# Kernel optimization log

Measured on AMD Instinct MI355X. Metric: run time of the kernel, lower is better.

## Reference

```python
import jax, jax.numpy as jnp
import numpy as np

EPS = 1e-6

def layernorm(x, alpha, bias):
    # torch.std default is unbiased (ddof=1)
    mean = x.mean(axis=-1, keepdims=True)
    std = jnp.std(x, axis=-1, keepdims=True, ddof=1)
    return alpha * (x - mean) / (std + EPS) + bias


def setup_inputs() -> dict:
    key = jax.random.key(0)
    B, L, d_model = 2, 1024, 1024
    d_state, d_conv, expand = 16, 4, 2
    d_inner = expand * d_model
    ks = jax.random.split(key, 8)
    std = 0.02
    x = jax.random.normal(ks[0], (B, L, d_model), dtype=jnp.float32)
    in_proj_w = jax.random.normal(ks[1], (2 * d_inner, d_model), dtype=jnp.float32) * std
    in_proj_b = jnp.zeros((2 * d_inner,), jnp.float32)
    conv_w = jax.random.normal(ks[2], (d_inner, 1, d_conv), dtype=jnp.float32) * std  # depthwise, groups=d_inner
    conv_b = jnp.zeros((d_inner,), jnp.float32)
    x_proj_w = jax.random.normal(ks[3], (2 * d_state, d_inner), dtype=jnp.float32) * std
    x_proj_b = jnp.zeros((2 * d_state,), jnp.float32)
    dt_proj_w = jax.random.normal(ks[4], (d_inner, d_inner), dtype=jnp.float32) * std
    dt_proj_b = jnp.zeros((d_inner,), jnp.float32)
    A_log = jnp.log(jnp.tile(jnp.arange(1, d_state + 1, dtype=jnp.float32), (d_inner, 1)))
    D = jnp.ones((d_inner,), jnp.float32)
    out_proj_w = jax.random.normal(ks[5], (d_model, d_inner), dtype=jnp.float32) * std
    out_proj_b = jnp.zeros((d_model,), jnp.float32)
    in_norm_alpha = jnp.ones((d_model,), jnp.float32)
    in_norm_bias = jnp.zeros((d_model,), jnp.float32)
    norm_alpha = jnp.ones((d_model,), jnp.float32)
    norm_bias = jnp.zeros((d_model,), jnp.float32)
    return {"x": x, "in_proj_w": in_proj_w, "in_proj_b": in_proj_b,
            "conv_w": conv_w, "conv_b": conv_b,
            "x_proj_w": x_proj_w, "x_proj_b": x_proj_b,
            "dt_proj_w": dt_proj_w, "dt_proj_b": dt_proj_b,
            "A_log": A_log, "D": D,
            "out_proj_w": out_proj_w, "out_proj_b": out_proj_b,
            "in_norm_alpha": in_norm_alpha, "in_norm_bias": in_norm_bias,
            "norm_alpha": norm_alpha, "norm_bias": norm_bias}


def reference(x, in_proj_w, in_proj_b, conv_w, conv_b, x_proj_w, x_proj_b,
              dt_proj_w, dt_proj_b, A_log, D, out_proj_w, out_proj_b,
              in_norm_alpha, in_norm_bias, norm_alpha, norm_bias):
    batch, L, d_model = x.shape
    d_inner = D.shape[0]
    d_state = A_log.shape[1]
    d_conv = conv_w.shape[-1]

    residual = x
    xn = layernorm(x, in_norm_alpha, in_norm_bias)
    xz = xn @ in_proj_w.T + in_proj_b                    # (B, L, 2*d_inner)
    x_in, z = jnp.split(xz, 2, axis=-1)

    # causal depthwise conv: torch pads both sides by d_conv-1 then slices [:L]
    # -> equivalent to left-pad only
    xc = jnp.swapaxes(x_in, 1, 2)                        # (B, d_inner, L)
    xc = jax.lax.conv_general_dilated(
        xc, conv_w, window_strides=(1,), padding=[(d_conv - 1, 0)],
        dimension_numbers=('NCH', 'OIH', 'NCH'),
        feature_group_count=d_inner) + conv_b[None, :, None]
    xc = jax.nn.silu(jnp.swapaxes(xc, 1, 2))             # (B, L, d_inner)

    Bmat, Cmat = jnp.split(xc @ x_proj_w.T + x_proj_b, 2, axis=-1)  # (B, L, d_state) each
    delta = jnp.clip(jax.nn.softplus(xc @ dt_proj_w.T + dt_proj_b), 1e-4, 10.0)
    A = -jnp.exp(A_log)                                  # (d_inner, d_state)
    flags = (jnp.arange(L) % 16) == 15                   # periodic renorm mask

    def step(h, inp):
        d_t, B_t, C_t, x_t, flag = inp                   # d_t,x_t: (B,d_inner); B_t,C_t: (B,d_state)
        dA = jnp.exp(jnp.clip(d_t[..., None] * A, -10.0, 0.0))      # (B,d_inner,d_state)
        dBx = d_t[..., None] * B_t[:, None, :] * x_t[..., None]
        h = dA * h + dBx
        hn = jnp.maximum(jnp.linalg.norm(h, axis=-1, keepdims=True), 1e-6)
        scale = jnp.where(hn > 10.0, 10.0 / hn, 1.0)
        h = jnp.where(flag, h * scale, h)
        y_t = jnp.sum(C_t[:, None, :] * h, axis=-1) + D * x_t
        return h, y_t

    h0 = jnp.zeros((batch, d_inner, d_state), dtype=x.dtype)
    xs = (jnp.swapaxes(delta, 0, 1), jnp.swapaxes(Bmat, 0, 1),
          jnp.swapaxes(Cmat, 0, 1), jnp.swapaxes(xc, 0, 1), flags)
    _, ys = jax.lax.scan(step, h0, xs)                   # ys: (L, B, d_inner)
    y = jnp.swapaxes(ys, 0, 1)

    y = y * jax.nn.silu(z)
    out = y @ out_proj_w.T + out_proj_b                  # dropout is identity in eval
    return layernorm(residual + out, norm_alpha, norm_bias)
```

## Files before the change

### kernel.cpp

```cpp
#include <hip/hip_runtime.h>
#include <math.h>

typedef unsigned short u16;
typedef unsigned int   u32;
typedef __bf16 bf16x8 __attribute__((ext_vector_type(8)));
typedef float  f32x4  __attribute__((ext_vector_type(4)));
typedef u16    u16x8  __attribute__((ext_vector_type(8)));

#define NB   2
#define LL   1024
#define DM   1024
#define DI   2048
#define MM   (NB*LL)
#define NXZ  (2*DI)
#define DSTATE 16
#define NSEG 64
#define NDT  2176
#define F32PAT 0x3F800000u

__device__ __forceinline__ float b2f(u16 u) {
  union { u32 i; float f; } v; v.i = ((u32)u) << 16; return v.f;
}
__device__ __forceinline__ u16 f2b(float f) {
  union { float f; u32 i; } v; v.f = f;
  u32 r = (v.i + 0x7FFFu + ((v.i >> 16) & 1u)) >> 16;
  return (u16)r;
}
__device__ __forceinline__ float ldx(const void* p, size_t i, bool isf32) {
  return isf32 ? ((const float*)p)[i] : b2f(((const u16*)p)[i]);
}
__device__ __forceinline__ float spclip(float v) {
  v = (v > 20.0f) ? v : __logf(1.0f + __expf(v));
  return fminf(fmaxf(v, 1e-4f), 10.0f);
}

typedef __attribute__((address_space(1))) const void gas_t;
typedef __attribute__((address_space(3))) void las_t;
__device__ __forceinline__ void gload_lds16(const void* g, void* l) {
  __builtin_amdgcn_global_load_lds((gas_t*)g, (las_t*)l, 16, 0, 0);
}

#define CVT_A  4194304u
#define CVT_B  8388608u
#define CVT_C 10485760u
#define CVT_D 10551296u
#define CVT_E 10747904u
#define CVT_BLOCKS 10496

__global__ __launch_bounds__(256) void cvtln_kernel(
    const void* __restrict__ s_in, const void* __restrict__ s_dt,
    const void* __restrict__ s_op, const void* __restrict__ s_xp,
    u16* __restrict__ inpw, u16* __restrict__ wdt, u16* __restrict__ opw,
    const void* __restrict__ x, const void* __restrict__ alpha,
    const void* __restrict__ beta, u16* __restrict__ xn,
    const u32* __restrict__ probe)
{
  const bool isf32 = (*probe == F32PAT);
  __shared__ float sb[4], ssb[4];
  if (blockIdx.x < CVT_BLOCKS) {
    size_t i4 = ((size_t)blockIdx.x * 256 + threadIdx.x) * 4;
    const void* src; u16* dst; size_t off;
    if      (i4 < CVT_A) { src = s_in; dst = inpw;        off = i4; }
    else if (i4 < CVT_B) { src = s_dt; dst = wdt;         off = i4 - CVT_A; }
    else if (i4 < CVT_C) { src = s_op; dst = opw;         off = i4 - CVT_B; }
    else if (i4 < CVT_D) { src = s_xp; dst = wdt + CVT_A; off = i4 - CVT_C; }
    else {
      ushort4 z = {0, 0, 0, 0};
      *(ushort4*)(wdt + 4259840u + (i4 - CVT_D)) = z;
      return;
    }
    ushort4 o;
    if (isf32) {
      float4 f = *(const float4*)((const float*)src + off);
      o.x = f2b(f.x); o.y = f2b(f.y); o.z = f2b(f.z); o.w = f2b(f.w);
    } else {
      o = *(const ushort4*)((const u16*)src + off);
    }
    *(ushort4*)(dst + off) = o;
    return;
  }
  int row = blockIdx.x - CVT_BLOCKS;
  int base = threadIdx.x * 4;
  size_t ix = (size_t)row * DM + base;
  float v0, v1, v2, v3;
  if (isf32) {
    float4 f = *(const float4*)((const float*)x + ix);
    v0 = f.x; v1 = f.y; v2 = f.z; v3 = f.w;
  } else {
    ushort4 u = *(const ushort4*)((const u16*)x + ix);
    v0 = b2f(u.x); v1 = b2f(u.y); v2 = b2f(u.z); v3 = b2f(u.w);
  }
  float s  = v0 + v1 + v2 + v3;
  float ss = v0*v0 + v1*v1 + v2*v2 + v3*v3;
#pragma unroll
  for (int off = 32; off > 0; off >>= 1) {
    s  += __shfl_down(s,  off);
    ss += __shfl_down(ss, off);
  }
  int wv = threadIdx.x >> 6, ln = threadIdx.x & 63;
  if (ln == 0) { sb[wv] = s; ssb[wv] = ss; }
  __syncthreads();
  s  = sb[0]  + sb[1]  + sb[2]  + sb[3];
  ss = ssb[0] + ssb[1] + ssb[2] + ssb[3];
  float mean = s * (1.0f / DM);
  float var  = fmaxf((ss - (float)DM * mean * mean) * (1.0f / (DM - 1)), 0.0f);
  float inv  = 1.0f / (sqrtf(var) + 1e-6f);
  float a0 = ldx(alpha, base+0, isf32), a1 = ldx(alpha, base+1, isf32);
  float a2 = ldx(alpha, base+2, isf32), a3 = ldx(alpha, base+3, isf32);
  float b0 = ldx(beta,  base+0, isf32), b1 = ldx(beta,  base+1, isf32);
  float b2 = ldx(beta,  base+2, isf32), b3 = ldx(beta,  base+3, isf32);
  ushort4 o;
  o.x = f2b(a0 * (v0 - mean) * inv + b0);
  o.y = f2b(a1 * (v1 - mean) * inv + b1);
  o.z = f2b(a2 * (v2 - mean) * inv + b2);
  o.w = f2b(a3 * (v3 - mean) * inv + b3);
  *(ushort4*)(xn + ix) = o;
}

__global__ __launch_bounds__(256) void ln1_kernel(
    const void* __restrict__ x, const void* __restrict__ alpha,
    const void* __restrict__ beta, u16* __restrict__ out,
    const u32* __restrict__ probe)
{
  const bool isf32 = (*probe == F32PAT);
  int row = blockIdx.x;
  int base = threadIdx.x * 4;
  size_t ix = (size_t)row * DM + base;
  float v0, v1, v2, v3;
  if (isf32) {
    float4 f = *(const float4*)((const float*)x + ix);
    v0 = f.x; v1 = f.y; v2 = f.z; v3 = f.w;
  } else {
    ushort4 u = *(const ushort4*)((const u16*)x + ix);
    v0 = b2f(u.x); v1 = b2f(u.y); v2 = b2f(u.z); v3 = b2f(u.w);
  }
  float s  = v0 + v1 + v2 + v3;
  float ss = v0*v0 + v1*v1 + v2*v2 + v3*v3;
#pragma unroll
  for (int off = 32; off > 0; off >>= 1) {
    s  += __shfl_down(s,  off);
    ss += __shfl_down(ss, off);
  }
  __shared__ float sb[4], ssb[4];
  int wv = threadIdx.x >> 6, ln = threadIdx.x & 63;
  if (ln == 0) { sb[wv] = s; ssb[wv] = ss; }
  __syncthreads();
  s  = sb[0]  + sb[1]  + sb[2]  + sb[3];
  ss = ssb[0] + ssb[1] + ssb[2] + ssb[3];
  float mean = s * (1.0f / DM);
  float var  = fmaxf((ss - (float)DM * mean * mean) * (1.0f / (DM - 1)), 0.0f);
  float inv  = 1.0f / (sqrtf(var) + 1e-6f);
  float a0 = ldx(alpha, base+0, isf32), a1 = ldx(alpha, base+1, isf32);
  float a2 = ldx(alpha, base+2, isf32), a3 = ldx(alpha, base+3, isf32);
  float b0 = ldx(beta,  base+0, isf32), b1 = ldx(beta,  base+1, isf32);
  float b2 = ldx(beta,  base+2, isf32), b3 = ldx(beta,  base+3, isf32);
  ushort4 o;
  o.x = f2b(a0 * (v0 - mean) * inv + b0);
  o.y = f2b(a1 * (v1 - mean) * inv + b1);
  o.z = f2b(a2 * (v2 - mean) * inv + b2);
  o.w = f2b(a3 * (v3 - mean) * inv + b3);
  *(ushort4*)(out + ix) = o;
}

__global__ __launch_bounds__(256) void ln2_kernel(
    const void* __restrict__ x, const float* __restrict__ outp,
    const void* __restrict__ alpha, const void* __restrict__ beta,
    void* __restrict__ out, const u32* __restrict__ probe)
{
  const bool isf32 = (*probe == F32PAT);
  int row = blockIdx.x;
  int base = threadIdx.x * 4;
  size_t ix = (size_t)row * DM + base;
  float v0, v1, v2, v3;
  if (isf32) {
    float4 f = *(const float4*)((const float*)x + ix);
    v0 = f.x; v1 = f.y; v2 = f.z; v3 = f.w;
  } else {
    ushort4 u = *(const ushort4*)((const u16*)x + ix);
    v0 = b2f(u.x); v1 = b2f(u.y); v2 = b2f(u.z); v3 = b2f(u.w);
  }
  float4 p = *(const float4*)(outp + ix);
  v0 += p.x; v1 += p.y; v2 += p.z; v3 += p.w;
  float s  = v0 + v1 + v2 + v3;
  float ss = v0*v0 + v1*v1 + v2*v2 + v3*v3;
#pragma unroll
  for (int off = 32; off > 0; off >>= 1) {
    s  += __shfl_down(s,  off);
    ss += __shfl_down(ss, off);
  }
  __shared__ float sb[4], ssb[4];
  int wv = threadIdx.x >> 6, ln = threadIdx.x & 63;
  if (ln == 0) { sb[wv] = s; ssb[wv] = ss; }
  __syncthreads();
  s  = sb[0]  + sb[1]  + sb[2]  + sb[3];
  ss = ssb[0] + ssb[1] + ssb[2] + ssb[3];
  float mean = s * (1.0f / DM);
  float var  = fmaxf((ss - (float)DM * mean * mean) * (1.0f / (DM - 1)), 0.0f);
  float inv  = 1.0f / (sqrtf(var) + 1e-6f);
  float a0 = ldx(alpha, base+0, isf32), a1 = ldx(alpha, base+1, isf32);
  float a2 = ldx(alpha, base+2, isf32), a3 = ldx(alpha, base+3, isf32);
  float b0 = ldx(beta,  base+0, isf32), b1 = ldx(beta,  base+1, isf32);
  float b2 = ldx(beta,  base+2, isf32), b3 = ldx(beta,  base+3, isf32);
  float r0 = a0 * (v0 - mean) * inv + b0;
  float r1 = a1 * (v1 - mean) * inv + b1;
  float r2 = a2 * (v2 - mean) * inv + b2;
  float r3 = a3 * (v3 - mean) * inv + b3;
  if (isf32) {
    float4 o; o.x = r0; o.y = r1; o.z = r2; o.w = r3;
    *(float4*)((float*)out + ix) = o;
  } else {
    ushort4 o; o.x = f2b(r0); o.y = f2b(r1); o.z = f2b(r2); o.w = f2b(r3);
    *(ushort4*)((u16*)out + ix) = o;
  }
}

__global__ __launch_bounds__(256) void ln2_sk_kernel(
    const void* __restrict__ x, const float* __restrict__ P,
    const void* __restrict__ op_bias,
    const void* __restrict__ alpha, const void* __restrict__ beta,
    void* __restrict__ out, const u32* __restrict__ probe)
{
  const bool isf32 = (*probe == F32PAT);
  int row = blockIdx.x;
  int base = threadIdx.x * 4;
  size_t ix = (size_t)row * DM + base;
  float v0, v1, v2, v3;
  if (isf32) {
    float4 f = *(const float4*)((const float*)x + ix);
    v0 = f.x; v1 = f.y; v2 = f.z; v3 = f.w;
  } else {
    ushort4 u = *(const ushort4*)((const u16*)x + ix);
    v0 = b2f(u.x); v1 = b2f(u.y); v2 = b2f(u.z); v3 = b2f(u.w);
  }
  v0 += ldx(op_bias, base+0, isf32);
  v1 += ldx(op_bias, base+1, isf32);
  v2 += ldx(op_bias, base+2, isf32);
  v3 += ldx(op_bias, base+3, isf32);
#pragma unroll
  for (int sk = 0; sk < 4; ++sk) {
    float4 p = *(const float4*)(P + ((size_t)sk * MM + row) * DM + base);
    v0 += p.x; v1 += p.y; v2 += p.z; v3 += p.w;
  }
  float s  = v0 + v1 + v2 + v3;
  float ss = v0*v0 + v1*v1 + v2*v2 + v3*v3;
#pragma unroll
  for (int off = 32; off > 0; off >>= 1) {
    s  += __shfl_down(s,  off);
    ss += __shfl_down(ss, off);
  }
  __shared__ float sb[4], ssb[4];
  int wv = threadIdx.x >> 6, ln = threadIdx.x & 63;
  if (ln == 0) { sb[wv] = s; ssb[wv] = ss; }
  __syncthreads();
  s  = sb[0]  + sb[1]  + sb[2]  + sb[3];
  ss = ssb[0] + ssb[1] + ssb[2] + ssb[3];
  float mean = s * (1.0f / DM);
  float var  = fmaxf((ss - (float)DM * mean * mean) * (1.0f / (DM - 1)), 0.0f);
  float inv  = 1.0f / (sqrtf(var) + 1e-6f);
  float a0 = ldx(alpha, base+0, isf32), a1 = ldx(alpha, base+1, isf32);
  float a2 = ldx(alpha, base+2, isf32), a3 = ldx(alpha, base+3, isf32);
  float b0 = ldx(beta,  base+0, isf32), b1 = ldx(beta,  base+1, isf32);
  float b2 = ldx(beta,  base+2, isf32), b3 = ldx(beta,  base+3, isf32);
  float r0 = a0 * (v0 - mean) * inv + b0;
  float r1 = a1 * (v1 - mean) * inv + b1;
  float r2 = a2 * (v2 - mean) * inv + b2;
  float r3 = a3 * (v3 - mean) * inv + b3;
  if (isf32) {
    float4 o; o.x = r0; o.y = r1; o.z = r2; o.w = r3;
    *(float4*)((float*)out + ix) = o;
  } else {
    ushort4 o; o.x = f2b(r0); o.y = f2b(r1); o.z = f2b(r2); o.w = f2b(r3);
    *(ushort4*)((u16*)out + ix) = o;
  }
}

__global__ __launch_bounds__(256) void cvt_kernel(
    const void* __restrict__ s_in, const void* __restrict__ s_dt,
    const void* __restrict__ s_op, const void* __restrict__ s_xp,
    u16* __restrict__ inpw, u16* __restrict__ wdt, u16* __restrict__ opw,
    const u32* __restrict__ probe)
{
  const bool isf32 = (*probe == F32PAT);
  size_t i4 = ((size_t)blockIdx.x * 256 + threadIdx.x) * 4;
  if (i4 >= CVT_E) return;
  const void* src; u16* dst; size_t off;
  if      (i4 < CVT_A) { src = s_in; dst = inpw;        off = i4; }
  else if (i4 < CVT_B) { src = s_dt; dst = wdt;         off = i4 - CVT_A; }
  else if (i4 < CVT_C) { src = s_op; dst = opw;         off = i4 - CVT_B; }
  else if (i4 < CVT_D) { src = s_xp; dst = wdt + CVT_A; off = i4 - CVT_C; }
  else {
    ushort4 z = {0, 0, 0, 0};
    *(ushort4*)(wdt + 4259840u + (i4 - CVT_D)) = z;
    return;
  }
  ushort4 o;
  if (isf32) {
    float4 f = *(const float4*)((const float*)src + off);
    o.x = f2b(f.x); o.y = f2b(f.y); o.z = f2b(f.z); o.w = f2b(f.w);
  } else {
    o = *(const ushort4*)((const u16*)src + off);
  }
  *(ushort4*)(dst + off) = o;
}

__device__ __forceinline__ void stage64(const u16* __restrict__ G, int rowK,
                                        int k0, u16* __restrict__ lds,
                                        int wave, int lane, int m0) {
#pragma unroll
  for (int q = 0; q < 4; ++q) {
    int ci = (wave * 4 + q) * 64 + lane;
    int r  = ci >> 3;
    int s  = ci & 7;
    int ch = s ^ (r & 7);
    const u16* ga = G + (size_t)(m0 + r) * rowK + k0 + ch * 8;
    gload_lds16(ga, lds + (size_t)ci * 8);
  }
}
__device__ __forceinline__ bf16x8 frag64(const u16* __restrict__ lds,
                                         int r, int ch) {
  int s = ch ^ (r & 7);
  return *(const bf16x8*)(lds + (size_t)r * 64 + s * 8);
}

#define EPI_NONE 0
#define EPI_SOFTPLUS 1

template<int EPI, int OUTBF>
__global__ __launch_bounds__(256) void gemm_fast(
    const u16* __restrict__ A, const u16* __restrict__ W,
    const void* __restrict__ bias, void* __restrict__ Cout,
    const u32* __restrict__ probe, int M, int N, int K)
{
  __shared__ __align__(16) u16 As[128 * 64];
  __shared__ __align__(16) u16 Ws[128 * 64];
  const bool isf32 = (*probe == F32PAT);
  const int tid  = threadIdx.x;
  const int wave = tid >> 6;
  const int lane = tid & 63;
  const int quad = lane >> 4;
  const int l16  = lane & 15;
  const int m0 = blockIdx.x * 128;
  const int n0 = blockIdx.y * 128;
  const int wm = (wave >> 1) * 64;
  const int wn = (wave & 1) * 64;

  f32x4 acc[4][4] = {};

  for (int k0 = 0; k0 < K; k0 += 64) {
    __syncthreads();
    stage64(A, K, k0, As, wave, lane, m0);
    stage64(W, K, k0, Ws, wave, lane, n0);
    __syncthreads();
#pragma unroll
    for (int kk = 0; kk < 2; ++kk) {
      bf16x8 af[4], bfr[4];
#pragma unroll
      for (int i = 0; i < 4; ++i) {
        af[i]  = frag64(As, wm + i * 16 + l16, kk * 4 + quad);
        bfr[i] = frag64(Ws, wn + i * 16 + l16, kk * 4 + quad);
      }
#pragma unroll
      for (int i = 0; i < 4; ++i)
#pragma unroll
        for (int j = 0; j < 4; ++j)
          acc[i][j] = __builtin_amdgcn_mfma_f32_16x16x32_bf16(af[i], bfr[j], acc[i][j], 0, 0, 0);
    }
  }

#pragma unroll
  for (int i = 0; i < 4; ++i) {
    int rbase = m0 + wm + i * 16 + quad * 4;
#pragma unroll
    for (int j = 0; j < 4; ++j) {
      int col = n0 + wn + j * 16 + l16;
      float bv = ldx(bias, col, isf32);
#pragma unroll
      for (int r = 0; r < 4; ++r) {
        float v = acc[i][j][r] + bv;
        if (EPI == EPI_SOFTPLUS) v = spclip(v);
        size_t oi = (size_t)(rbase + r) * N + col;
        if (OUTBF) ((u16*)Cout)[oi] = f2b(v);
        else       ((float*)Cout)[oi] = v;
      }
    }
  }
}

template<int PARTBF>
__global__ __launch_bounds__(256) void gemm_sk(
    const u16* __restrict__ A, const u16* __restrict__ W,
    void* __restrict__ P, int M, int N, int Kfull, int Kslice)
{
  __shared__ __align__(16) u16 As[128 * 64];
  __shared__ __align__(16) u16 Ws[128 * 64];
  const int tid  = threadIdx.x;
  const int wave = tid >> 6;
  const int lane = tid & 63;
  const int quad = lane >> 4;
  const int l16  = lane & 15;
  const int m0 = blockIdx.x * 128;
  const int n0 = blockIdx.y * 128;
  const int sk = blockIdx.z;
  const int kbeg = sk * Kslice;
  const int kend = kbeg + Kslice;
  const int wm = (wave >> 1) * 64;
  const int wn = (wave & 1) * 64;

  f32x4 acc[4][4] = {};

  for (int k0 = kbeg; k0 < kend; k0 += 64) {
    __syncthreads();
    stage64(A, Kfull, k0, As, wave, lane, m0);
    stage64(W, Kfull, k0, Ws, wave, lane, n0);
    __syncthreads();
#pragma unroll
    for (int kk = 0; kk < 2; ++kk) {
      bf16x8 af[4], bfr[4];
#pragma unroll
      for (int i = 0; i < 4; ++i) {
        af[i]  = frag64(As, wm + i * 16 + l16, kk * 4 + quad);
        bfr[i] = frag64(Ws, wn + i * 16 + l16, kk * 4 + quad);
      }
#pragma unroll
      for (int i = 0; i < 4; ++i)
#pragma unroll
        for (int j = 0; j < 4; ++j)
          acc[i][j] = __builtin_amdgcn_mfma_f32_16x16x32_bf16(af[i], bfr[j], acc[i][j], 0, 0, 0);
    }
  }

#pragma unroll
  for (int i = 0; i < 4; ++i) {
    int rbase = m0 + wm + i * 16 + quad * 4;
#pragma unroll
    for (int j = 0; j < 4; ++j) {
      int col = n0 + wn + j * 16 + l16;
#pragma unroll
      for (int r = 0; r < 4; ++r) {
        size_t oi = (size_t)sk * M * N + (size_t)(rbase + r) * N + col;
        if (PARTBF) ((u16*)P)[oi] = f2b(acc[i][j][r]);
        else        ((float*)P)[oi] = acc[i][j][r];
      }
    }
  }
}

template<int EPI, int OUTBF>
__global__ __launch_bounds__(256) void gemm_r2(
    const u16* __restrict__ A, const void* __restrict__ W,
    const void* __restrict__ bias, void* __restrict__ Cout,
    const u32* __restrict__ probe, int M, int N, int K)
{
  __shared__ __align__(16) u16 As[128 * 32];
  __shared__ __align__(16) u16 Ws[128 * 32];
  const bool isf32 = (*probe == F32PAT);
  const int tid  = threadIdx.x;
  const int wave = tid >> 6;
  const int lane = tid & 63;
  const int quad = lane >> 4;
  const int l16  = lane & 15;
  const int m0 = blockIdx.x * 128;
  const int n0 = blockIdx.y * 128;
  const int wm = (wave >> 1) * 64;
  const int wn = (wave & 1) * 64;

  f32x4 acc[4][4] = {};

  for (int k0 = 0; k0 < K; k0 += 32) {
    u16x8 va[2], vw[2];
#pragma unroll
    for (int q = 0; q < 2; ++q) {
      int ci  = wave * 128 + q * 64 + lane;
      int row = ci >> 2;
      int kc  = (ci & 3) * 8;
      va[q] = *(const u16x8*)(A + (size_t)(m0 + row) * K + k0 + kc);
      size_t wi = (size_t)(n0 + row) * K + k0 + kc;
      if (isf32) {
        const float* Wf = (const float*)W;
        float4 f0 = *(const float4*)(Wf + wi);
        float4 f1 = *(const float4*)(Wf + wi + 4);
        u16x8 t;
        t[0] = f2b(f0.x); t[1] = f2b(f0.y); t[2] = f2b(f0.z); t[3] = f2b(f0.w);
        t[4] = f2b(f1.x); t[5] = f2b(f1.y); t[6] = f2b(f1.z); t[7] = f2b(f1.w);
        vw[q] = t;
      } else {
        vw[q] = *(const u16x8*)((const u16*)W + wi);
      }
    }
    __syncthreads();
#pragma unroll
    for (int q = 0; q < 2; ++q) {
      int ci = wave * 128 + q * 64 + lane;
      *(u16x8*)(As + (size_t)ci * 8) = va[q];
      *(u16x8*)(Ws + (size_t)ci * 8) = vw[q];
    }
    __syncthreads();
    bf16x8 af[4], bfr[4];
#pragma unroll
    for (int i = 0; i < 4; ++i) {
      af[i]  = *(const bf16x8*)(As + (size_t)(wm + i * 16 + l16) * 32 + quad * 8);
      bfr[i] = *(const bf16x8*)(Ws + (size_t)(wn + i * 16 + l16) * 32 + quad * 8);
    }
#pragma unroll
    for (int i = 0; i < 4; ++i)
#pragma unroll
      for (int j = 0; j < 4; ++j)
        acc[i][j] = __builtin_amdgcn_mfma_f32_16x16x32_bf16(af[i], bfr[j], acc[i][j], 0, 0, 0);
  }

#pragma unroll
  for (int i = 0; i < 4; ++i) {
    int rbase = m0 + wm + i * 16 + quad * 4;
#pragma unroll
    for (int j = 0; j < 4; ++j) {
      int col = n0 + wn + j * 16 + l16;
      float bv = ldx(bias, col, isf32);
#pragma unroll
      for (int r = 0; r < 4; ++r) {
        float v = acc[i][j][r] + bv;
        if (EPI == EPI_SOFTPLUS) v = spclip(v);
        size_t oi = (size_t)(rbase + r) * N + col;
        if (OUTBF) ((u16*)Cout)[oi] = f2b(v);
        else       ((float*)Cout)[oi] = v;
      }
    }
  }
}

__global__ __launch_bounds__(256) void conv_silu_kernel(
    const u16* __restrict__ xz, const void* __restrict__ cw,
    const void* __restrict__ cb, u16* __restrict__ xc_bf,
    const u32* __restrict__ probe)
{
  const bool isf32 = (*probe == F32PAT);
  int g = blockIdx.x * 256 + threadIdx.x;
  int c = g & (DI - 1);
  int m = g >> 11;
  int l = m & (LL - 1);
  float w0 = ldx(cw, c*4+0, isf32), w1 = ldx(cw, c*4+1, isf32);
  float w2 = ldx(cw, c*4+2, isf32), w3 = ldx(cw, c*4+3, isf32);
  const u16* col = xz + (size_t)m * NXZ + c;
  float acc = ldx(cb, c, isf32);
  acc += w3 * b2f(col[0]);
  if (l >= 1) acc += w2 * b2f(*(col - NXZ));
  if (l >= 2) acc += w1 * b2f(*(col - 2*NXZ));
  if (l >= 3) acc += w0 * b2f(*(col - 3*NXZ));
  float sil = acc / (1.0f + __expf(-acc));
  xc_bf[g] = f2b(sil);
}

__global__ __launch_bounds__(256) void proj_bc_r2(
    const u16* __restrict__ xc, const void* __restrict__ W,
    const void* __restrict__ bias, float* __restrict__ bc,
    const u32* __restrict__ probe)
{
  const bool isf32 = (*probe == F32PAT);
  int m = blockIdx.x;
  int n = threadIdx.x >> 3;
  int part = threadIdx.x & 7;
  const u16* xr = xc + (size_t)m * DI + part * 256;
  size_t wbase = (size_t)n * DI + part * 256;
  float acc = 0.0f;
  if (isf32) {
    const float* wr = (const float*)W + wbase;
#pragma unroll 8
    for (int i = 0; i < 256; i += 4) {
      ushort4 xv = *(const ushort4*)(xr + i);
      float4  wv = *(const float4*)(wr + i);
      acc += b2f(xv.x)*wv.x + b2f(xv.y)*wv.y + b2f(xv.z)*wv.z + b2f(xv.w)*wv.w;
    }
  } else {
    const u16* wr = (const u16*)W + wbase;
#pragma unroll 8
    for (int i = 0; i < 256; i += 4) {
      ushort4 xv = *(const ushort4*)(xr + i);
      ushort4 wv = *(const ushort4*)(wr + i);
      acc += b2f(xv.x)*b2f(wv.x) + b2f(xv.y)*b2f(wv.y)
           + b2f(xv.z)*b2f(wv.z) + b2f(xv.w)*b2f(wv.w);
    }
  }
  __shared__ float ps[256];
  ps[threadIdx.x] = acc;
  __syncthreads();
  if (threadIdx.x < 32) {
    float s = 0.0f;
#pragma unroll
    for (int p = 0; p < 8; ++p) s += ps[threadIdx.x * 8 + p];
    bc[(size_t)m * 32 + threadIdx.x] = s + ldx(bias, threadIdx.x, isf32);
  }
}

__global__ __launch_bounds__(256, 4) void scan_p1(
    const u16* __restrict__ Pdt, const void* __restrict__ bias_dt,
    const void* __restrict__ bias_xp,
    const u16* __restrict__ xc, const void* __restrict__ A_log,
    float2* __restrict__ PQ, const u32* __restrict__ probe)
{
  const bool isf32 = (*probe == F32PAT);
  const int c = blockIdx.x * 256 + threadIdx.x;
  const int g = blockIdx.y;
  const int b = blockIdx.z;
  const int row0 = b * LL + g * 16;
  const u16* P0 = Pdt;
  const u16* P1 = Pdt + (size_t)MM * NDT;
  __shared__ float sBC[512];
  if (threadIdx.x < 128) {
    int j = threadIdx.x >> 3, k0 = (threadIdx.x & 7) * 4;
    size_t base = (size_t)(row0 + j) * NDT + DI + k0;
#pragma unroll
    for (int i = 0; i < 4; ++i)
      sBC[j * 32 + k0 + i] = b2f(P0[base + i]) + b2f(P1[base + i])
                           + ldx(bias_xp, k0 + i, isf32);
  }
  float Av2[16];
#pragma unroll
  for (int s = 0; s < 16; ++s)
    Av2[s] = -__expf(ldx(A_log, (size_t)c * DSTATE + s, isf32)) * 1.44269504f;
  const float bdt = ldx(bias_dt, c, isf32);
  float p[16], q[16];
#pragma unroll
  for (int s = 0; s < 16; ++s) { p[s] = 1.0f; q[s] = 0.0f; }
  __syncthreads();
  const float CLIP2 = -14.4269504f;
#pragma unroll 4
  for (int j = 0; j < 16; ++j) {
    int row = row0 + j;
    size_t pi = (size_t)row * NDT + c;
    float d  = spclip(b2f(P0[pi]) + b2f(P1[pi]) + bdt);
    float x  = b2f(xc[(size_t)row * DI + c]);
    float dx = d * x;
    float4 B4[4];
    B4[0] = *(const float4*)&sBC[j * 32 + 0];
    B4[1] = *(const float4*)&sBC[j * 32 + 4];
    B4[2] = *(const float4*)&sBC[j * 32 + 8];
    B4[3] = *(const float4*)&sBC[j * 32 + 12];
    const float* Bv = (const float*)B4;
#pragma unroll
    for (int s = 0; s < 16; ++s) {
      float a = __builtin_amdgcn_exp2f(fmaxf(d * Av2[s], CLIP2));
      q[s] = a * q[s] + dx * Bv[s];
      p[s] *= a;
    }
  }
  float2* out = PQ + ((size_t)(b * NSEG + g) * DI + c) * DSTATE;
#pragma unroll
  for (int s = 0; s < 16; ++s) out[s] = make_float2(p[s], q[s]);
}

__global__ __launch_bounds__(256) void scan_p2(
    const float2* __restrict__ PQ, u16* __restrict__ Hin,
    float* __restrict__ Scale)
{
  const int s = threadIdx.x & 15;
  const int c = blockIdx.x * 16 + (threadIdx.x >> 4);
  const int b = blockIdx.y;
  const size_t stride = (size_t)DI * DSTATE;
  const size_t base = ((size_t)b * NSEG * DI + c) * DSTATE + s;
  float h = 0.0f;
  float2 pq = PQ[base];
  for (int g = 0; g < NSEG; ++g) {
    float2 cur = pq;
    if (g < NSEG - 1) pq = PQ[base + (size_t)(g + 1) * stride];
    Hin[base + (size_t)g * stride] = f2b(h);
    h = cur.x * h + cur.y;
    float n2 = h * h;
    n2 += __shfl_xor(n2, 1);
    n2 += __shfl_xor(n2, 2);
    n2 += __shfl_xor(n2, 4);
    n2 += __shfl_xor(n2, 8);
    float hn = fmaxf(sqrtf(n2), 1e-6f);
    float sc = hn > 10.0f ? 10.0f / hn : 1.0f;
    if (s == 0) Scale[((size_t)b * NSEG + g) * DI + c] = sc;
    h *= sc;
  }
}

__global__ __launch_bounds__(256, 4) void scan_p3(
    const u16* __restrict__ Pdt, const void* __restrict__ bias_dt,
    const void* __restrict__ bias_xp,
    const u16* __restrict__ xc, const u16* __restrict__ xz,
    const void* __restrict__ A_log, const void* __restrict__ Dp,
    const u16* __restrict__ Hin, const float* __restrict__ Scale,
    u16* __restrict__ y_bf, const u32* __restrict__ probe)
{
  const bool isf32 = (*probe == F32PAT);
  const int c = blockIdx.x * 256 + threadIdx.x;
  const int g = blockIdx.y;
  const int b = blockIdx.z;
  const int row0 = b * LL + g * 16;
  const u16* P0 = Pdt;
  const u16* P1 = Pdt + (size_t)MM * NDT;
  __shared__ float sBC[512];
  if (threadIdx.x < 128) {
    int j = threadIdx.x >> 3, k0 = (threadIdx.x & 7) * 4;
    size_t base = (size_t)(row0 + j) * NDT + DI + k0;
#pragma unroll
    for (int i = 0; i < 4; ++i)
      sBC[j * 32 + k0 + i] = b2f(P0[base + i]) + b2f(P1[base + i])
                           + ldx(bias_xp, k0 + i, isf32);
  }
  float Av2[16];
#pragma unroll
  for (int s = 0; s < 16; ++s)
    Av2[s] = -__expf(ldx(A_log, (size_t)c * DSTATE + s, isf32)) * 1.44269504f;
  const float bdt = ldx(bias_dt, c, isf32);
  float h[16];
  const u16* hp = Hin + ((size_t)(b * NSEG + g) * DI + c) * DSTATE;
  {
    u16x8 h0 = *(const u16x8*)(hp);
    u16x8 h1 = *(const u16x8*)(hp + 8);
#pragma unroll
    for (int s = 0; s < 8; ++s) { h[s] = b2f(h0[s]); h[8 + s] = b2f(h1[s]); }
  }
  const float sc15 = Scale[((size_t)b * NSEG + g) * DI + c];
  const float Dc = ldx(Dp, c, isf32);
  __syncthreads();
  const float CLIP2 = -14.4269504f;
#pragma unroll 4
  for (int j = 0; j < 16; ++j) {
    int row = row0 + j;
    size_t pi = (size_t)row * NDT + c;
    float d  = spclip(b2f(P0[pi]) + b2f(P1[pi]) + bdt);
    float x  = b2f(xc[(size_t)row * DI + c]);
    float z  = b2f(xz[(size_t)row * NXZ + DI + c]);
    float dx = d * x;
    float4 BC[8];
    BC[0] = *(const float4*)&sBC[j * 32 + 0];
    BC[1] = *(const float4*)&sBC[j * 32 + 4];
    BC[2] = *(const float4*)&sBC[j * 32 + 8];
    BC[3] = *(const float4*)&sBC[j * 32 + 12];
    BC[4] = *(const float4*)&sBC[j * 32 + 16];
    BC[5] = *(const float4*)&sBC[j * 32 + 20];
    BC[6] = *(const float4*)&sBC[j * 32 + 24];
    BC[7] = *(const float4*)&sBC[j * 32 + 28];
    const float* Bv = (const float*)BC;
    const float* Cv = Bv + 16;
#pragma unroll
    for (int s = 0; s < 16; ++s) {
      float a = __builtin_amdgcn_exp2f(fmaxf(d * Av2[s], CLIP2));
      h[s] = a * h[s] + dx * Bv[s];
    }
    if (j == 15) {
#pragma unroll
      for (int s = 0; s < 16; ++s) h[s] *= sc15;
    }
    float ys = 0.0f;
#pragma unroll
    for (int s = 0; s < 16; ++s) ys += Cv[s] * h[s];
    float yo = (ys + Dc * x) * (z / (1.0f + __expf(-z)));
    y_bf[(size_t)row * DI + c] = f2b(yo);
  }
}

__global__ __launch_bounds__(256) void scan_mono(
    const float* __restrict__ delta, const float* __restrict__ bc,
    const u16* __restrict__ xc, const u16* __restrict__ xz,
    const void* __restrict__ A_log, const void* __restrict__ Dp,
    u16* __restrict__ y_bf, const u32* __restrict__ probe)
{
  const bool isf32 = (*probe == F32PAT);
  const int s = threadIdx.x & 15;
  const int c = blockIdx.x * 16 + (threadIdx.x >> 4);
  const int b = blockIdx.y;
  const float Av2 = -__expf(ldx(A_log, (size_t)c * DSTATE + s, isf32)) * 1.44269504f;
  const float Dc  = ldx(Dp, c, isf32);
  const float CLIP2 = -14.4269504f;
  float h = 0.0f;
  for (int t0 = 0; t0 < LL; t0 += 16) {
    float dl[16], xl[16], zl[16], Bv[16], Cv[16];
#pragma unroll
    for (int j = 0; j < 16; ++j) {
      int row = b * LL + t0 + j;
      dl[j] = delta[(size_t)row * DI + c];
      xl[j] = b2f(xc[(size_t)row * DI + c]);
      zl[j] = b2f(xz[(size_t)row * NXZ + DI + c]);
      Bv[j] = bc[(size_t)row * 32 + s];
      Cv[j] = bc[(size_t)row * 32 + 16 + s];
    }
#pragma unroll
    for (int j = 0; j < 16; ++j) {
      float d = dl[j], x = xl[j];
      float dA = __builtin_amdgcn_exp2f(fmaxf(d * Av2, CLIP2));
      h = dA * h + (d * x) * Bv[j];
      if (j == 15) {
        float n2 = h * h;
        n2 += __shfl_xor(n2, 1); n2 += __shfl_xor(n2, 2);
        n2 += __shfl_xor(n2, 4); n2 += __shfl_xor(n2, 8);
        float hn = fmaxf(sqrtf(n2), 1e-6f);
        float sc = hn > 10.0f ? 10.0f / hn : 1.0f;
        h *= sc;
      }
      float ys = Cv[j] * h;
      ys += __shfl_xor(ys, 1); ys += __shfl_xor(ys, 2);
      ys += __shfl_xor(ys, 4); ys += __shfl_xor(ys, 8);
      float z = zl[j];
      float yo = (ys + Dc * x) * (z / (1.0f + __expf(-z)));
      if (s == 0) {
        int row = b * LL + t0 + j;
        y_bf[(size_t)row * DI + c] = f2b(yo);
      }
    }
  }
}

extern "C" void kernel_launch(void* const* d_in, const int* in_sizes, int n_in,
                              void* d_out, int out_size, void* d_ws, size_t ws_size,
                              hipStream_t stream) {
  const void* x          = d_in[0];
  const void* in_proj_w  = d_in[1];
  const void* in_proj_b  = d_in[2];
  const void* conv_w     = d_in[3];
  const void* conv_b     = d_in[4];
  const void* x_proj_w   = d_in[5];
  const void* x_proj_b   = d_in[6];
  const void* dt_proj_w  = d_in[7];
  const void* dt_proj_b  = d_in[8];
  const void* A_log      = d_in[9];
  const void* Dp         = d_in[10];
  const void* out_proj_w = d_in[11];
  const void* out_proj_b = d_in[12];
  const void* in_norm_a  = d_in[13];
  const void* in_norm_b  = d_in[14];
  const void* norm_a     = d_in[15];
  const void* norm_b     = d_in[16];
  const u32*  probe      = (const u32*)d_in[13];

  const size_t MiB = 1048576;
  const size_t NEED_NEW = 106299392;

  if (ws_size >= NEED_NEW) {
    char* w = (char*)d_ws;
    u16*   xz_bf = (u16*)w;    w += 16 * MiB;
    u16*   xc_bf = (u16*)w;    w += 8 * MiB;
    u16*   Pdt   = (u16*)w;    w += 17 * MiB;
    float* Scale = (float*)w;  w += 1 * MiB;
    u16*   opw   = (u16*)w;    w += 4 * MiB;
    u16*   y_bf  = (u16*)w;    w += 8 * MiB;
    char* S = w;
    u16*    inpw   = (u16*)(S);
    u16*    wdt    = (u16*)(S + 8*MiB);
    u16*    xn_bf  = (u16*)(S + 16*MiB + 512*1024);
    float2* PQ     = (float2*)(S);
    u16*    Hin    = (u16*)(S + 32*MiB);
    float*  outP   = (float*)(S);

    cvtln_kernel<<<CVT_BLOCKS + MM, 256, 0, stream>>>(
        in_proj_w, dt_proj_w, out_proj_w, x_proj_w, inpw, wdt, opw,
        x, in_norm_a, in_norm_b, xn_bf, probe);
    gemm_fast<EPI_NONE, 1><<<dim3(MM/128, NXZ/128), 256, 0, stream>>>(
        xn_bf, inpw, in_proj_b, xz_bf, probe, MM, NXZ, DM);
    conv_silu_kernel<<<(MM * DI) / 256, 256, 0, stream>>>(xz_bf, conv_w, conv_b, xc_bf, probe);
    gemm_sk<1><<<dim3(MM/128, NDT/128, 2), 256, 0, stream>>>(
        xc_bf, wdt, Pdt, MM, NDT, DI, DI/2);
    scan_p1<<<dim3(DI/256, NSEG, NB), 256, 0, stream>>>(
        Pdt, dt_proj_b, x_proj_b, xc_bf, A_log, PQ, probe);
    scan_p2<<<dim3(DI/16, NB), 256, 0, stream>>>(PQ, Hin, Scale);
    scan_p3<<<dim3(DI/256, NSEG, NB), 256, 0, stream>>>(
        Pdt, dt_proj_b, x_proj_b, xc_bf, xz_bf, A_log, Dp, Hin, Scale, y_bf, probe);
    gemm_sk<0><<<dim3(MM/128, DM/128, 4), 256, 0, stream>>>(
        y_bf, opw, outP, MM, DM, DI, DI/4);
    ln2_sk_kernel<<<MM, 256, 0, stream>>>(x, outP, out_proj_b, norm_a, norm_b, d_out, probe);
  } else {
    char* w = (char*)d_ws;
    u16*   xn_bf = (u16*)w;   w += (size_t)MM * DM * 2;
    u16*   xz_bf = (u16*)w;   w += (size_t)MM * NXZ * 2;
    u16*   xc_bf = (u16*)w;   w += (size_t)MM * DI * 2;
    float* delta = (float*)w; w += (size_t)MM * DI * 4;
    float* bc    = (float*)w; w += (size_t)MM * 32 * 4;
    u16*   y_bf  = (u16*)w;   w += (size_t)MM * DI * 2;
    float* outp  = (float*)w; w += (size_t)MM * DM * 4;

    ln1_kernel<<<MM, 256, 0, stream>>>(x, in_norm_a, in_norm_b, xn_bf, probe);
    gemm_r2<EPI_NONE, 1><<<dim3(MM/128, NXZ/128), 256, 0, stream>>>(
        xn_bf, in_proj_w, in_proj_b, xz_bf, probe, MM, NXZ, DM);
    conv_silu_kernel<<<(MM * DI) / 256, 256, 0, stream>>>(xz_bf, conv_w, conv_b, xc_bf, probe);
    gemm_r2<EPI_SOFTPLUS, 0><<<dim3(MM/128, DI/128), 256, 0, stream>>>(
        xn_bf == 0 ? xc_bf : xc_bf, dt_proj_w, dt_proj_b, delta, probe, MM, DI, DI);
    proj_bc_r2<<<MM, 256, 0, stream>>>(xc_bf, x_proj_w, x_proj_b, bc, probe);
    scan_mono<<<dim3(DI/16, NB), 256, 0, stream>>>(delta, bc, xc_bf, xz_bf, A_log, Dp, y_bf, probe);
    gemm_r2<EPI_NONE, 0><<<dim3(MM/128, DM/128), 256, 0, stream>>>(
        y_bf, out_proj_w, out_proj_b, outp, probe, MM, DM, DI);
    ln2_kernel<<<MM, 256, 0, stream>>>(x, outp, norm_a, norm_b, d_out, probe);
  }
}
```

Before: 315.1 us.

## Split-K all GEMMs with bf16 partials and fold bias into consumers

Replaces the in_proj GEMM with a 2-way split-K GEMM that writes bf16 partial planes. The conv and scan_p3 kernels now sum those partials and add the in_proj bias themselves. The dt/x_proj GEMM goes from 2-way to 4-way split-K, and out_proj partials are stored as bf16 instead of fp32 before the final layernorm sums them. The aim is more blocks in flight for the 16x16-tile GEMMs and less partial-buffer traffic. In exchange, consumers read more partial planes, the workspace requirement grows to 172 MiB, and bf16 rounding of partials may reduce accuracy.

```diff
diff --git a/kernel.cpp b/kernel.cpp
--- a/kernel.cpp
+++ b/kernel.cpp
@@ -214,8 +214,8 @@
   }
 }
 
-__global__ __launch_bounds__(256) void ln2_sk_kernel(
-    const void* __restrict__ x, const float* __restrict__ P,
+__global__ __launch_bounds__(256) void ln2_skb_kernel(
+    const void* __restrict__ x, const u16* __restrict__ P,
     const void* __restrict__ op_bias,
     const void* __restrict__ alpha, const void* __restrict__ beta,
     void* __restrict__ out, const u32* __restrict__ probe)
@@ -238,8 +238,8 @@
   v3 += ldx(op_bias, base+3, isf32);
 #pragma unroll
   for (int sk = 0; sk < 4; ++sk) {
-    float4 p = *(const float4*)(P + ((size_t)sk * MM + row) * DM + base);
-    v0 += p.x; v1 += p.y; v2 += p.z; v3 += p.w;
+    ushort4 p = *(const ushort4*)(P + ((size_t)sk * MM + row) * DM + base);
+    v0 += b2f(p.x); v1 += b2f(p.y); v2 += b2f(p.z); v3 += b2f(p.w);
   }
   float s  = v0 + v1 + v2 + v3;
   float ss = v0*v0 + v1*v1 + v2*v2 + v3*v3;
@@ -274,35 +274,6 @@
   }
 }
 
-__global__ __launch_bounds__(256) void cvt_kernel(
-    const void* __restrict__ s_in, const void* __restrict__ s_dt,
-    const void* __restrict__ s_op, const void* __restrict__ s_xp,
-    u16* __restrict__ inpw, u16* __restrict__ wdt, u16* __restrict__ opw,
-    const u32* __restrict__ probe)
-{
-  const bool isf32 = (*probe == F32PAT);
-  size_t i4 = ((size_t)blockIdx.x * 256 + threadIdx.x) * 4;
-  if (i4 >= CVT_E) return;
-  const void* src; u16* dst; size_t off;
-  if      (i4 < CVT_A) { src = s_in; dst = inpw;        off = i4; }
-  else if (i4 < CVT_B) { src = s_dt; dst = wdt;         off = i4 - CVT_A; }
-  else if (i4 < CVT_C) { src = s_op; dst = opw;         off = i4 - CVT_B; }
-  else if (i4 < CVT_D) { src = s_xp; dst = wdt + CVT_A; off = i4 - CVT_C; }
-  else {
-    ushort4 z = {0, 0, 0, 0};
-    *(ushort4*)(wdt + 4259840u + (i4 - CVT_D)) = z;
-    return;
-  }
-  ushort4 o;
-  if (isf32) {
-    float4 f = *(const float4*)((const float*)src + off);
-    o.x = f2b(f.x); o.y = f2b(f.y); o.z = f2b(f.z); o.w = f2b(f.w);
-  } else {
-    o = *(const ushort4*)((const u16*)src + off);
-  }
-  *(ushort4*)(dst + off) = o;
-}
-
 __device__ __forceinline__ void stage64(const u16* __restrict__ G, int rowK,
                                         int k0, u16* __restrict__ lds,
                                         int wave, int lane, int m0) {
@@ -322,74 +293,9 @@
   return *(const bf16x8*)(lds + (size_t)r * 64 + s * 8);
 }
 
-#define EPI_NONE 0
-#define EPI_SOFTPLUS 1
-
-template<int EPI, int OUTBF>
-__global__ __launch_bounds__(256) void gemm_fast(
-    const u16* __restrict__ A, const u16* __restrict__ W,
-    const void* __restrict__ bias, void* __restrict__ Cout,
-    const u32* __restrict__ probe, int M, int N, int K)
-{
-  __shared__ __align__(16) u16 As[128 * 64];
-  __shared__ __align__(16) u16 Ws[128 * 64];
-  const bool isf32 = (*probe == F32PAT);
-  const int tid  = threadIdx.x;
-  const int wave = tid >> 6;
-  const int lane = tid & 63;
-  const int quad = lane >> 4;
-  const int l16  = lane & 15;
-  const int m0 = blockIdx.x * 128;
-  const int n0 = blockIdx.y * 128;
-  const int wm = (wave >> 1) * 64;
-  const int wn = (wave & 1) * 64;
-
-  f32x4 acc[4][4] = {};
-
-  for (int k0 = 0; k0 < K; k0 += 64) {
-    __syncthreads();
-    stage64(A, K, k0, As, wave, lane, m0);
-    stage64(W, K, k0, Ws, wave, lane, n0);
-    __syncthreads();
-#pragma unroll
-    for (int kk = 0; kk < 2; ++kk) {
-      bf16x8 af[4], bfr[4];
-#pragma unroll
-      for (int i = 0; i < 4; ++i) {
-        af[i]  = frag64(As, wm + i * 16 + l16, kk * 4 + quad);
-        bfr[i] = frag64(Ws, wn + i * 16 + l16, kk * 4 + quad);
-      }
-#pragma unroll
-      for (int i = 0; i < 4; ++i)
-#pragma unroll
-        for (int j = 0; j < 4; ++j)
-          acc[i][j] = __builtin_amdgcn_mfma_f32_16x16x32_bf16(af[i], bfr[j], acc[i][j], 0, 0, 0);
-    }
-  }
-
-#pragma unroll
-  for (int i = 0; i < 4; ++i) {
-    int rbase = m0 + wm + i * 16 + quad * 4;
-#pragma unroll
-    for (int j = 0; j < 4; ++j) {
-      int col = n0 + wn + j * 16 + l16;
-      float bv = ldx(bias, col, isf32);
-#pragma unroll
-      for (int r = 0; r < 4; ++r) {
-        float v = acc[i][j][r] + bv;
-        if (EPI == EPI_SOFTPLUS) v = spclip(v);
-        size_t oi = (size_t)(rbase + r) * N + col;
-        if (OUTBF) ((u16*)Cout)[oi] = f2b(v);
-        else       ((float*)Cout)[oi] = v;
-      }
-    }
-  }
-}
-
-template<int PARTBF>
 __global__ __launch_bounds__(256) void gemm_sk(
     const u16* __restrict__ A, const u16* __restrict__ W,
-    void* __restrict__ P, int M, int N, int Kfull, int Kslice)
+    u16* __restrict__ P, int M, int N, int Kfull, int Kslice)
 {
   __shared__ __align__(16) u16 As[128 * 64];
   __shared__ __align__(16) u16 Ws[128 * 64];
@@ -429,6 +335,7 @@
     }
   }
 
+  u16* Pb = P + (size_t)sk * M * N;
 #pragma unroll
   for (int i = 0; i < 4; ++i) {
     int rbase = m0 + wm + i * 16 + quad * 4;
@@ -436,14 +343,14 @@
     for (int j = 0; j < 4; ++j) {
       int col = n0 + wn + j * 16 + l16;
 #pragma unroll
-      for (int r = 0; r < 4; ++r) {
-        size_t oi = (size_t)sk * M * N + (size_t)(rbase + r) * N + col;
-        if (PARTBF) ((u16*)P)[oi] = f2b(acc[i][j][r]);
-        else        ((float*)P)[oi] = acc[i][j][r];
-      }
-    }
-  }
-}
+      for (int r = 0; r < 4; ++r)
+        Pb[(size_t)(rbase + r) * N + col] = f2b(acc[i][j][r]);
+    }
+  }
+}
+
+#define EPI_NONE 0
+#define EPI_SOFTPLUS 1
 
 template<int EPI, int OUTBF>
 __global__ __launch_bounds__(256) void gemm_r2(
@@ -527,6 +434,30 @@
   }
 }
 
+__global__ __launch_bounds__(256) void conv_silu_p_kernel(
+    const u16* __restrict__ Pxz, const void* __restrict__ ipb,
+    const void* __restrict__ cw, const void* __restrict__ cb,
+    u16* __restrict__ xc_bf, const u32* __restrict__ probe)
+{
+  const bool isf32 = (*probe == F32PAT);
+  int g = blockIdx.x * 256 + threadIdx.x;
+  int c = g & (DI - 1);
+  int m = g >> 11;
+  int l = m & (LL - 1);
+  const u16* X0 = Pxz + (size_t)m * NXZ + c;
+  const u16* X1 = X0 + (size_t)MM * NXZ;
+  const float bx = ldx(ipb, c, isf32);
+  float w0 = ldx(cw, c*4+0, isf32), w1 = ldx(cw, c*4+1, isf32);
+  float w2 = ldx(cw, c*4+2, isf32), w3 = ldx(cw, c*4+3, isf32);
+  float acc = ldx(cb, c, isf32);
+  acc += w3 * (b2f(X0[0]) + b2f(X1[0]) + bx);
+  if (l >= 1) acc += w2 * (b2f(*(X0 - NXZ))   + b2f(*(X1 - NXZ))   + bx);
+  if (l >= 2) acc += w1 * (b2f(*(X0 - 2*NXZ)) + b2f(*(X1 - 2*NXZ)) + bx);
+  if (l >= 3) acc += w0 * (b2f(*(X0 - 3*NXZ)) + b2f(*(X1 - 3*NXZ)) + bx);
+  float sil = acc / (1.0f + __expf(-acc));
+  xc_bf[g] = f2b(sil);
+}
+
 __global__ __launch_bounds__(256) void conv_silu_kernel(
     const u16* __restrict__ xz, const void* __restrict__ cw,
     const void* __restrict__ cb, u16* __restrict__ xc_bf,
@@ -590,6 +521,11 @@
   }
 }
 
+__device__ __forceinline__ float sum4(const u16* __restrict__ P, size_t i,
+                                      size_t plane) {
+  return b2f(P[i]) + b2f(P[i + plane]) + b2f(P[i + 2*plane]) + b2f(P[i + 3*plane]);
+}
+
 __global__ __launch_bounds__(256, 4) void scan_p1(
     const u16* __restrict__ Pdt, const void* __restrict__ bias_dt,
     const void* __restrict__ bias_xp,
@@ -601,15 +537,14 @@
   const int g = blockIdx.y;
   const int b = blockIdx.z;
   const int row0 = b * LL + g * 16;
-  const u16* P0 = Pdt;
-  const u16* P1 = Pdt + (size_t)MM * NDT;
+  const size_t plane = (size_t)MM * NDT;
   __shared__ float sBC[512];
   if (threadIdx.x < 128) {
     int j = threadIdx.x >> 3, k0 = (threadIdx.x & 7) * 4;
     size_t base = (size_t)(row0 + j) * NDT + DI + k0;
 #pragma unroll
     for (int i = 0; i < 4; ++i)
-      sBC[j * 32 + k0 + i] = b2f(P0[base + i]) + b2f(P1[base + i])
+      sBC[j * 32 + k0 + i] = sum4(Pdt, base + i, plane)
                            + ldx(bias_xp, k0 + i, isf32);
   }
   float Av2[16];
@@ -625,8 +560,7 @@
 #pragma unroll 4
   for (int j = 0; j < 16; ++j) {
     int row = row0 + j;
-    size_t pi = (size_t)row * NDT + c;
-    float d  = spclip(b2f(P0[pi]) + b2f(P1[pi]) + bdt);
+    float d  = spclip(sum4(Pdt, (size_t)row * NDT + c, plane) + bdt);
     float x  = b2f(xc[(size_t)row * DI + c]);
     float dx = d * x;
     float4 B4[4];
@@ -678,7 +612,8 @@
 __global__ __launch_bounds__(256, 4) void scan_p3(
     const u16* __restrict__ Pdt, const void* __restrict__ bias_dt,
     const void* __restrict__ bias_xp,
-    const u16* __restrict__ xc, const u16* __restrict__ xz,
+    const u16* __restrict__ xc, const u16* __restrict__ Pxz,
+    const void* __restrict__ ipb,
     const void* __restrict__ A_log, const void* __restrict__ Dp,
     const u16* __restrict__ Hin, const float* __restrict__ Scale,
     u16* __restrict__ y_bf, const u32* __restrict__ probe)
@@ -688,15 +623,15 @@
   const int g = blockIdx.y;
   const int b = blockIdx.z;
   const int row0 = b * LL + g * 16;
-  const u16* P0 = Pdt;
-  const u16* P1 = Pdt + (size_t)MM * NDT;
+  const size_t plane = (size_t)MM * NDT;
+  const size_t zplane = (size_t)MM * NXZ;
   __shared__ float sBC[512];
   if (threadIdx.x < 128) {
     int j = threadIdx.x >> 3, k0 = (threadIdx.x & 7) * 4;
     size_t base = (size_t)(row0 + j) * NDT + DI + k0;
 #pragma unroll
     for (int i = 0; i < 4; ++i)
-      sBC[j * 32 + k0 + i] = b2f(P0[base + i]) + b2f(P1[base + i])
+      sBC[j * 32 + k0 + i] = sum4(Pdt, base + i, plane)
                            + ldx(bias_xp, k0 + i, isf32);
   }
   float Av2[16];
@@ -704,6 +639,7 @@
   for (int s = 0; s < 16; ++s)
     Av2[s] = -__expf(ldx(A_log, (size_t)c * DSTATE + s, isf32)) * 1.44269504f;
   const float bdt = ldx(bias_dt, c, isf32);
+  const float bz  = ldx(ipb, DI + c, isf32);
   float h[16];
   const u16* hp = Hin + ((size_t)(b * NSEG + g) * DI + c) * DSTATE;
   {
@@ -719,10 +655,10 @@
 #pragma unroll 4
   for (int j = 0; j < 16; ++j) {
     int row = row0 + j;
-    size_t pi = (size_t)row * NDT + c;
-    float d  = spclip(b2f(P0[pi]) + b2f(P1[pi]) + bdt);
+    float d  = spclip(sum4(Pdt, (size_t)row * NDT + c, plane) + bdt);
     float x  = b2f(xc[(size_t)row * DI + c]);
-    float z  = b2f(xz[(size_t)row * NXZ + DI + c]);
+    size_t zi = (size_t)row * NXZ + DI + c;
+    float z  = b2f(Pxz[zi]) + b2f(Pxz[zi + zplane]) + bz;
     float dx = d * x;
     float4 BC[8];
     BC[0] = *(const float4*)&sBC[j * 32 + 0];
@@ -826,40 +762,41 @@
   const u32*  probe      = (const u32*)d_in[13];
 
   const size_t MiB = 1048576;
-  const size_t NEED_NEW = 106299392;
+  const size_t NEED_NEW = 172 * MiB;
 
   if (ws_size >= NEED_NEW) {
     char* w = (char*)d_ws;
-    u16*   xz_bf = (u16*)w;    w += 16 * MiB;
-    u16*   xc_bf = (u16*)w;    w += 8 * MiB;
-    u16*   Pdt   = (u16*)w;    w += 17 * MiB;
-    float* Scale = (float*)w;  w += 1 * MiB;
-    u16*   opw   = (u16*)w;    w += 4 * MiB;
-    u16*   y_bf  = (u16*)w;    w += 8 * MiB;
-    char* S = w;
-    u16*    inpw   = (u16*)(S);
-    u16*    wdt    = (u16*)(S + 8*MiB);
-    u16*    xn_bf  = (u16*)(S + 16*MiB + 512*1024);
-    float2* PQ     = (float2*)(S);
-    u16*    Hin    = (u16*)(S + 32*MiB);
-    float*  outP   = (float*)(S);
+    u16* inpw  = (u16*)w;  w += 8 * MiB;
+    u16* wdt   = (u16*)w;  w += 8 * MiB + 512 * 1024;
+    u16* opw   = (u16*)w;  w += 4 * MiB;
+    u16* xn_bf = (u16*)w;  w += 4 * MiB;
+    u16* Pxz   = (u16*)w;  w += 32 * MiB;
+    u16* xc_bf = (u16*)w;  w += 8 * MiB;
+    u16* Pdt   = (u16*)w;  w += 34 * MiB;
+    float2* PQ = (float2*)w; w += 32 * MiB;
+    u16* Hin   = (u16*)w;  w += 8 * MiB;
+    float* Scale = (float*)w; w += 1 * MiB;
+    u16* y_bf  = (u16*)w;  w += 8 * MiB;
+    u16* outPb = (u16*)w;  w += 16 * MiB;
 
     cvtln_kernel<<<CVT_BLOCKS + MM, 256, 0, stream>>>(
         in_proj_w, dt_proj_w, out_proj_w, x_proj_w, inpw, wdt, opw,
         x, in_norm_a, in_norm_b, xn_bf, probe);
-    gemm_fast<EPI_NONE, 1><<<dim3(MM/128, NXZ/128), 256, 0, stream>>>(
-        xn_bf, inpw, in_proj_b, xz_bf, probe, MM, NXZ, DM);
-    conv_silu_kernel<<<(MM * DI) / 256, 256, 0, stream>>>(xz_bf, conv_w, conv_b, xc_bf, probe);
-    gemm_sk<1><<<dim3(MM/128, NDT/128, 2), 256, 0, stream>>>(
-        xc_bf, wdt, Pdt, MM, NDT, DI, DI/2);
+    gemm_sk<<<dim3(MM/128, NXZ/128, 2), 256, 0, stream>>>(
+        xn_bf, inpw, Pxz, MM, NXZ, DM, DM/2);
+    conv_silu_p_kernel<<<(MM * DI) / 256, 256, 0, stream>>>(
+        Pxz, in_proj_b, conv_w, conv_b, xc_bf, probe);
+    gemm_sk<<<dim3(MM/128, NDT/128, 4), 256, 0, stream>>>(
+        xc_bf, wdt, Pdt, MM, NDT, DI, DI/4);
     scan_p1<<<dim3(DI/256, NSEG, NB), 256, 0, stream>>>(
         Pdt, dt_proj_b, x_proj_b, xc_bf, A_log, PQ, probe);
     scan_p2<<<dim3(DI/16, NB), 256, 0, stream>>>(PQ, Hin, Scale);
     scan_p3<<<dim3(DI/256, NSEG, NB), 256, 0, stream>>>(
-        Pdt, dt_proj_b, x_proj_b, xc_bf, xz_bf, A_log, Dp, Hin, Scale, y_bf, probe);
-    gemm_sk<0><<<dim3(MM/128, DM/128, 4), 256, 0, stream>>>(
-        y_bf, opw, outP, MM, DM, DI, DI/4);
-    ln2_sk_kernel<<<MM, 256, 0, stream>>>(x, outP, out_proj_b, norm_a, norm_b, d_out, probe);
+        Pdt, dt_proj_b, x_proj_b, xc_bf, Pxz, in_proj_b,
+        A_log, Dp, Hin, Scale, y_bf, probe);
+    gemm_sk<<<dim3(MM/128, DM/128, 4), 256, 0, stream>>>(
+        y_bf, opw, outPb, MM, DM, DI, DI/4);
+    ln2_skb_kernel<<<MM, 256, 0, stream>>>(x, outPb, out_proj_b, norm_a, norm_b, d_out, probe);
   } else {
     char* w = (char*)d_ws;
     u16*   xn_bf = (u16*)w;   w += (size_t)MM * DM * 2;
@@ -875,7 +812,7 @@
         xn_bf, in_proj_w, in_proj_b, xz_bf, probe, MM, NXZ, DM);
     conv_silu_kernel<<<(MM * DI) / 256, 256, 0, stream>>>(xz_bf, conv_w, conv_b, xc_bf, probe);
     gemm_r2<EPI_SOFTPLUS, 0><<<dim3(MM/128, DI/128), 256, 0, stream>>>(
-        xn_bf == 0 ? xc_bf : xc_bf, dt_proj_w, dt_proj_b, delta, probe, MM, DI, DI);
+        xc_bf, dt_proj_w, dt_proj_b, delta, probe, MM, DI, DI);
     proj_bc_r2<<<MM, 256, 0, stream>>>(xc_bf, x_proj_w, x_proj_b, bc, probe);
     scan_mono<<<dim3(DI/16, NB), 256, 0, stream>>>(delta, bc, xc_bf, xz_bf, A_log, Dp, y_bf, probe);
     gemm_r2<EPI_NONE, 0><<<dim3(MM/128, DM/128), 256, 0, stream>>>(
```

Measured after the change: 327.8 us. +4.0%, slower.
